# Kernel optimization log

Hardware: AMD Instinct MI355X
Metric: run time of the kernel (lower is better)

Reference implementation:

```python
import jax, jax.numpy as jnp
import numpy as np

D_MODEL = 1024
N_HEADS = 16
HEAD_DIM = D_MODEL // N_HEADS


def setup_inputs() -> dict:
    key = jax.random.key(0)
    ks = jax.random.split(key, 5)
    B, T = 2, 2048
    x = jax.random.normal(ks[0], (B, T, D_MODEL), dtype=jnp.float32)
    s_in = 1.0 / np.sqrt(D_MODEL)
    W_qkv = jax.random.normal(ks[1], (D_MODEL, 3 * D_MODEL), dtype=jnp.float32) * s_in
    b_qkv = jnp.zeros((3 * D_MODEL,), dtype=jnp.float32)
    W_out = jax.random.normal(ks[2], (D_MODEL, D_MODEL), dtype=jnp.float32) * s_in
    b_out = jnp.zeros((D_MODEL,), dtype=jnp.float32)
    return {"x": x, "W_qkv": W_qkv, "b_qkv": b_qkv, "W_out": W_out, "b_out": b_out}


def reference(x, W_qkv, b_qkv, W_out, b_out):
    B, T, C = x.shape
    qkv = x @ W_qkv + b_qkv  # (B, T, 3C)
    q, k, v = jnp.split(qkv, 3, axis=-1)
    # (B, H, T, Dh)
    q = q.reshape(B, T, N_HEADS, HEAD_DIM).transpose(0, 2, 1, 3)
    k = k.reshape(B, T, N_HEADS, HEAD_DIM).transpose(0, 2, 1, 3)
    v = v.reshape(B, T, N_HEADS, HEAD_DIM).transpose(0, 2, 1, 3)
    scale = 1.0 / jnp.sqrt(jnp.asarray(HEAD_DIM, dtype=x.dtype))
    scores = jnp.einsum('bhqd,bhkd->bhqk', q, k) * scale  # (B, H, T, T)
    causal = jnp.tril(jnp.ones((T, T), dtype=bool))
    scores = jnp.where(causal[None, None], scores, jnp.asarray(-jnp.inf, dtype=scores.dtype))
    attn = jax.nn.softmax(scores, axis=-1)
    out = jnp.einsum('bhqk,bhkd->bhqd', attn, v)  # (B, H, T, Dh)
    out = out.transpose(0, 2, 1, 3).reshape(B, T, C)
    return out @ W_out + b_out
```

## Files before the change

kernel.cpp:

```cpp
#include <hip/hip_runtime.h>
#include <hip/hip_bf16.h>
#include <stdint.h>

typedef __bf16 bf16;
typedef __bf16 bf16x4 __attribute__((ext_vector_type(4)));
typedef __bf16 bf16x8 __attribute__((ext_vector_type(8)));
typedef float  f32x4  __attribute__((ext_vector_type(4)));

#define D_MODEL 1024
#define N_HEADS 16
#define HEAD_DIM 64
#define SEQ 2048
#define BATCH 2
#define LOG2E 1.4426950408889634f
#define NEG_SENT -3.0e4f
#define CAP 24.0f

__device__ __forceinline__ bf16x8 ld8(const bf16* p) { return *(const bf16x8*)p; }

__device__ __forceinline__ void async16(const bf16* g, bf16* l) {
  __builtin_amdgcn_global_load_lds(
      (const __attribute__((address_space(1))) void*)g,
      (__attribute__((address_space(3))) void*)l, 16, 0, 0);
}

__global__ __launch_bounds__(256)
void prep(const float* __restrict__ x, bf16* __restrict__ x16,
          const float* __restrict__ Wqkv, bf16* __restrict__ Wqkv_t,
          const float* __restrict__ Wout, bf16* __restrict__ Wout_t) {
  __shared__ float tile[32][33];
  const int blk = blockIdx.x, tid = threadIdx.x;
  if (blk < 4096) {
    int i = (blk * 256 + tid) * 4;
    float4 v = *(const float4*)&x[i];
    bf16 o[4] = {(bf16)v.x, (bf16)v.y, (bf16)v.z, (bf16)v.w};
    *(uint2*)&x16[i] = *(uint2*)o;
    return;
  }
  const float* in; bf16* out; int R, C, c0, r0;
  if (blk < 7168) {
    int b = blk - 4096;
    in = Wqkv; out = Wqkv_t; R = 1024; C = 3072;
    c0 = (b % 96) * 32; r0 = (b / 96) * 32;
  } else {
    int b = blk - 7168;
    in = Wout; out = Wout_t; R = 1024; C = 1024;
    c0 = (b % 32) * 32; r0 = (b / 32) * 32;
  }
  const int tx = tid & 31, ty = tid >> 5;
  #pragma unroll
  for (int i = 0; i < 32; i += 8)
    tile[ty + i][tx] = in[(size_t)(r0 + ty + i) * C + c0 + tx];
  __syncthreads();
  #pragma unroll
  for (int i = 0; i < 32; i += 8)
    out[(size_t)(c0 + ty + i) * R + r0 + tx] = (bf16)tile[tx][ty + i];
}

__global__ __launch_bounds__(256)
void gemm_bt(const bf16* __restrict__ A, const bf16* __restrict__ Bt,
             const float* __restrict__ bias, float* __restrict__ outf,
             bf16* __restrict__ Qp, bf16* __restrict__ Kp, bf16* __restrict__ Vtp,
             int N, int mode) {
  __shared__ __align__(16) bf16 shA[128 * 32];
  __shared__ __align__(16) bf16 shB[128 * 32];
  const int tid  = threadIdx.x;
  const int bm0  = blockIdx.y * 128, bn0 = blockIdx.x * 128;
  const int wave = tid >> 6, lane = tid & 63;
  const int quad = lane >> 4, l16 = lane & 15;
  const int wm = (wave >> 1) * 64, wn = (wave & 1) * 64;

  const int c_lo  = tid;
  const int row_lo = c_lo >> 2,  col_lo = (c_lo & 3) << 3;
  const int c_hi  = tid + 256;
  const int row_hi = c_hi >> 2,  col_hi = (c_hi & 3) << 3;
  const int cb_lo = (wave * 64) * 8;
  const int cb_hi = (256 + wave * 64) * 8;

  f32x4 acc[4][4];
  #pragma unroll
  for (int i = 0; i < 4; i++)
    #pragma unroll
    for (int j = 0; j < 4; j++)
      acc[i][j] = (f32x4){0.f, 0.f, 0.f, 0.f};

  for (int k0 = 0; k0 < 1024; k0 += 32) {
    async16(&A[(size_t)(bm0 + row_lo) * 1024 + k0 + col_lo], &shA[cb_lo]);
    async16(&A[(size_t)(bm0 + row_hi) * 1024 + k0 + col_hi], &shA[cb_hi]);
    async16(&Bt[(size_t)(bn0 + row_lo) * 1024 + k0 + col_lo], &shB[cb_lo]);
    async16(&Bt[(size_t)(bn0 + row_hi) * 1024 + k0 + col_hi], &shB[cb_hi]);
    __syncthreads();
    bf16x8 af[4], bg[4];
    #pragma unroll
    for (int i = 0; i < 4; i++)
      af[i] = ld8(&shA[(wm + i * 16 + l16) * 32 + quad * 8]);
    #pragma unroll
    for (int j = 0; j < 4; j++)
      bg[j] = ld8(&shB[(wn + j * 16 + l16) * 32 + quad * 8]);
    #pragma unroll
    for (int i = 0; i < 4; i++)
      #pragma unroll
      for (int j = 0; j < 4; j++)
        acc[i][j] = __builtin_amdgcn_mfma_f32_16x16x32_bf16(af[i], bg[j], acc[i][j], 0, 0, 0);
    __syncthreads();
  }

  #pragma unroll
  for (int i = 0; i < 4; i++) {
    #pragma unroll
    for (int j = 0; j < 4; j++) {
      int gn = bn0 + wn + j * 16 + l16;
      float bv = bias[gn];
      #pragma unroll
      for (int r = 0; r < 4; r++) {
        int gm = bm0 + wm + i * 16 + quad * 4 + r;
        float v = acc[i][j][r] + bv;
        if (mode == 1) {
          outf[(size_t)gm * N + gn] = v;
        } else {
          int which = gn >> 10, rem = gn & 1023;
          int h = rem >> 6, d = rem & 63;
          int b = gm >> 11, t = gm & 2047;
          int bh = b * N_HEADS + h;
          if (which == 0)      Qp[((size_t)bh * SEQ + t) * 64 + d]  = (bf16)v;
          else if (which == 1) Kp[((size_t)bh * SEQ + t) * 64 + d]  = (bf16)v;
          else                 Vtp[((size_t)bh * 64 + d) * SEQ + t] = (bf16)v;
        }
      }
    }
  }
}

__global__ __launch_bounds__(256)
void attn_k(const bf16* __restrict__ Qp, const bf16* __restrict__ Kp,
            const bf16* __restrict__ Vtp, bf16* __restrict__ Obuf) {
  __shared__ __align__(16) bf16 shK[64 * 64];
  __shared__ __align__(16) bf16 shV[64 * 64];
  __shared__ __align__(16) bf16 shPT[4][16 * 72];
  const int tid  = threadIdx.x;
  const int wave = tid >> 6, lane = tid & 63;
  const int quad = lane >> 4, l16 = lane & 15;
  const int bh = blockIdx.y, bx = blockIdx.x;
  const int qb = (bx & 1) ? (31 - (bx >> 1)) : (bx >> 1);
  const int qw0 = qb * 64 + wave * 16;

  const bf16* Qbh = Qp  + (size_t)bh * SEQ * 64;
  const bf16* Kbh = Kp  + (size_t)bh * SEQ * 64;
  const bf16* Vbh = Vtp + (size_t)bh * 64 * SEQ;

  const int lr3 = lane >> 3;
  const int swc = (lane & 7) ^ lr3;

  bf16x8 aQ[2];
  #pragma unroll
  for (int p = 0; p < 2; p++)
    aQ[p] = ld8(&Qbh[(size_t)(qw0 + l16) * 64 + p * 32 + quad * 8]);

  f32x4 o[4];
  #pragma unroll
  for (int j = 0; j < 4; j++) o[j] = (f32x4){0.f, 0.f, 0.f, 0.f};
  f32x4 lacc = (f32x4){0.f, 0.f, 0.f, 0.f};
  const int qlane = qw0 + l16;
  const int xq = l16 & 7;

  const float SC = 0.125f * LOG2E;
  const int LT = qb;
  bf16* PT = shPT[wave];

  for (int kt = 0; kt <= LT; kt++) {
    const int kbase = kt * 64;
    __syncthreads();
    #pragma unroll
    for (int s = 0; s < 2; s++) {
      int i = wave * 2 + s;
      int row = i * 8 + lr3;
      async16(&Kbh[(size_t)(kbase + row) * 64 + swc * 8], &shK[i * 512]);
      async16(&Vbh[(size_t)row * SEQ + kbase + swc * 8], &shV[i * 512]);
    }
    __syncthreads();
    if (kbase > qw0 + 15) continue;

    f32x4 st[4];
    #pragma unroll
    for (int c = 0; c < 4; c++) {
      bf16x8 kf0 = ld8(&shK[(c * 16 + l16) * 64 + ((quad    ) ^ xq) * 8]);
      bf16x8 kf1 = ld8(&shK[(c * 16 + l16) * 64 + ((quad + 4) ^ xq) * 8]);
      f32x4 acc = (f32x4){0.f, 0.f, 0.f, 0.f};
      acc = __builtin_amdgcn_mfma_f32_16x16x32_bf16(kf0, aQ[0], acc, 0, 0, 0);
      acc = __builtin_amdgcn_mfma_f32_16x16x32_bf16(kf1, aQ[1], acc, 0, 0, 0);
      st[c] = acc;
    }

    if (kbase + 63 > qw0) {
      #pragma unroll
      for (int c = 0; c < 4; c++)
        #pragma unroll
        for (int r = 0; r < 4; r++) {
          int key = kbase + c * 16 + quad * 4 + r;
          if (key > qlane) st[c][r] = NEG_SENT;
        }
    }

    #pragma unroll
    for (int c = 0; c < 4; c++) {
      #pragma unroll
      for (int r = 0; r < 4; r++)
        st[c][r] = exp2f(__builtin_fmaf(st[c][r], SC, -CAP));
      lacc += st[c];
    }

    #pragma unroll
    for (int c = 0; c < 4; c++) {
      bf16x4 pv = {(bf16)st[c][0], (bf16)st[c][1], (bf16)st[c][2], (bf16)st[c][3]};
      *(bf16x4*)&PT[l16 * 72 + c * 16 + quad * 4] = pv;
    }
    asm volatile("s_waitcnt lgkmcnt(0)" ::: "memory");
    bf16x8 bP0 = ld8(&PT[l16 * 72 + quad * 8]);
    bf16x8 bP1 = ld8(&PT[l16 * 72 + 32 + quad * 8]);

    #pragma unroll
    for (int j = 0; j < 4; j++) {
      bf16x8 v0 = ld8(&shV[(j * 16 + l16) * 64 + ((quad    ) ^ xq) * 8]);
      bf16x8 v1 = ld8(&shV[(j * 16 + l16) * 64 + ((quad + 4) ^ xq) * 8]);
      o[j] = __builtin_amdgcn_mfma_f32_16x16x32_bf16(v0, bP0, o[j], 0, 0, 0);
      o[j] = __builtin_amdgcn_mfma_f32_16x16x32_bf16(v1, bP1, o[j], 0, 0, 0);
    }
  }

  float lrow = (lacc[0] + lacc[1]) + (lacc[2] + lacc[3]);
  lrow += __shfl_xor(lrow, 16, 64);
  lrow += __shfl_xor(lrow, 32, 64);

  const int b = bh >> 4, h = bh & 15;
  {
    float inv = 1.0f / lrow;
    int t = qw0 + l16;
    size_t base = ((size_t)(b * SEQ + t)) * D_MODEL + h * 64;
    #pragma unroll
    for (int j = 0; j < 4; j++) {
      bf16x4 ov = {(bf16)(o[j][0] * inv), (bf16)(o[j][1] * inv),
                   (bf16)(o[j][2] * inv), (bf16)(o[j][3] * inv)};
      *(bf16x4*)&Obuf[base + j * 16 + quad * 4] = ov;
    }
  }
}

extern "C" void kernel_launch(void* const* d_in, const int* in_sizes, int n_in,
                              void* d_out, int out_size, void* d_ws, size_t ws_size,
                              hipStream_t stream) {
  const float* x    = (const float*)d_in[0];
  const float* Wqkv = (const float*)d_in[1];
  const float* bqkv = (const float*)d_in[2];
  const float* Wout = (const float*)d_in[3];
  const float* bout = (const float*)d_in[4];
  float* out = (float*)d_out;

  char* ws = (char*)d_ws;
  bf16* x16    = (bf16*)(ws);
  bf16* Wqkv_t = (bf16*)(ws + 8388608);
  bf16* Wout_t = (bf16*)(ws + 14680064);
  bf16* Qp     = (bf16*)(ws + 16777216);
  bf16* Kp     = (bf16*)(ws + 25165824);
  bf16* Vtp    = (bf16*)(ws + 33554432);
  bf16* Obuf   = x16;

  prep<<<8192, 256, 0, stream>>>(x, x16, Wqkv, Wqkv_t, Wout, Wout_t);

  gemm_bt<<<dim3(3072 / 128, 4096 / 128), 256, 0, stream>>>(
      x16, Wqkv_t, bqkv, nullptr, Qp, Kp, Vtp, 3072, 0);

  attn_k<<<dim3(32, BATCH * N_HEADS), 256, 0, stream>>>(Qp, Kp, Vtp, Obuf);

  gemm_bt<<<dim3(1024 / 128, 4096 / 128), 256, 0, stream>>>(
      Obuf, Wout_t, bout, out, nullptr, nullptr, nullptr, 1024, 1);
}
```

Before: 220.6 us.

## Load 128-key K/V tiles per barrier pair and vectorize V-transpose epilogue stores

The attention kernel now stages 128 keys of K and V into shared memory per iteration and processes them as two 64-key halves. This halves the number of block-wide barrier pairs and global-to-LDS load rounds. The cost is doubled LDS use, which can lower occupancy, plus extra wasted loads on the diagonal tile. The QKV GEMM epilogue also writes the transposed V output as 4-wide bf16 vectors instead of scalar stores.

```diff
diff --git a/kernel.cpp b/kernel.cpp
--- a/kernel.cpp
+++ b/kernel.cpp
@@ -111,20 +111,25 @@
     for (int j = 0; j < 4; j++) {
       int gn = bn0 + wn + j * 16 + l16;
       float bv = bias[gn];
-      #pragma unroll
-      for (int r = 0; r < 4; r++) {
-        int gm = bm0 + wm + i * 16 + quad * 4 + r;
-        float v = acc[i][j][r] + bv;
-        if (mode == 1) {
-          outf[(size_t)gm * N + gn] = v;
+      int gm0 = bm0 + wm + i * 16 + quad * 4;
+      if (mode == 1) {
+        #pragma unroll
+        for (int r = 0; r < 4; r++)
+          outf[(size_t)(gm0 + r) * N + gn] = acc[i][j][r] + bv;
+      } else {
+        int which = gn >> 10, rem = gn & 1023;
+        int h = rem >> 6, d = rem & 63;
+        int b = gm0 >> 11, t0 = gm0 & 2047;
+        int bh = b * N_HEADS + h;
+        if (which == 2) {
+          bf16x4 vv = {(bf16)(acc[i][j][0] + bv), (bf16)(acc[i][j][1] + bv),
+                       (bf16)(acc[i][j][2] + bv), (bf16)(acc[i][j][3] + bv)};
+          *(bf16x4*)&Vtp[((size_t)bh * 64 + d) * SEQ + t0] = vv;
         } else {
-          int which = gn >> 10, rem = gn & 1023;
-          int h = rem >> 6, d = rem & 63;
-          int b = gm >> 11, t = gm & 2047;
-          int bh = b * N_HEADS + h;
-          if (which == 0)      Qp[((size_t)bh * SEQ + t) * 64 + d]  = (bf16)v;
-          else if (which == 1) Kp[((size_t)bh * SEQ + t) * 64 + d]  = (bf16)v;
-          else                 Vtp[((size_t)bh * 64 + d) * SEQ + t] = (bf16)v;
+          bf16* dst = (which == 0) ? Qp : Kp;
+          #pragma unroll
+          for (int r = 0; r < 4; r++)
+            dst[((size_t)bh * SEQ + t0 + r) * 64 + d] = (bf16)(acc[i][j][r] + bv);
         }
       }
     }
@@ -134,8 +139,8 @@
 __global__ __launch_bounds__(256)
 void attn_k(const bf16* __restrict__ Qp, const bf16* __restrict__ Kp,
             const bf16* __restrict__ Vtp, bf16* __restrict__ Obuf) {
-  __shared__ __align__(16) bf16 shK[64 * 64];
-  __shared__ __align__(16) bf16 shV[64 * 64];
+  __shared__ __align__(16) bf16 shK[128 * 64];
+  __shared__ __align__(16) bf16 shV[64 * 128];
   __shared__ __align__(16) bf16 shPT[4][16 * 72];
   const int tid  = threadIdx.x;
   const int wave = tid >> 6, lane = tid & 63;
@@ -148,9 +153,6 @@
   const bf16* Kbh = Kp  + (size_t)bh * SEQ * 64;
   const bf16* Vbh = Vtp + (size_t)bh * 64 * SEQ;
 
-  const int lr3 = lane >> 3;
-  const int swc = (lane & 7) ^ lr3;
-
   bf16x8 aQ[2];
   #pragma unroll
   for (int p = 0; p < 2; p++)
@@ -164,66 +166,81 @@
   const int xq = l16 & 7;
 
   const float SC = 0.125f * LOG2E;
-  const int LT = qb;
+  const int NT = qb >> 1;
   bf16* PT = shPT[wave];
 
-  for (int kt = 0; kt <= LT; kt++) {
-    const int kbase = kt * 64;
-    __syncthreads();
-    #pragma unroll
-    for (int s = 0; s < 2; s++) {
-      int i = wave * 2 + s;
-      int row = i * 8 + lr3;
-      async16(&Kbh[(size_t)(kbase + row) * 64 + swc * 8], &shK[i * 512]);
-      async16(&Vbh[(size_t)row * SEQ + kbase + swc * 8], &shV[i * 512]);
-    }
-    __syncthreads();
-    if (kbase > qw0 + 15) continue;
-
-    f32x4 st[4];
-    #pragma unroll
-    for (int c = 0; c < 4; c++) {
-      bf16x8 kf0 = ld8(&shK[(c * 16 + l16) * 64 + ((quad    ) ^ xq) * 8]);
-      bf16x8 kf1 = ld8(&shK[(c * 16 + l16) * 64 + ((quad + 4) ^ xq) * 8]);
-      f32x4 acc = (f32x4){0.f, 0.f, 0.f, 0.f};
-      acc = __builtin_amdgcn_mfma_f32_16x16x32_bf16(kf0, aQ[0], acc, 0, 0, 0);
-      acc = __builtin_amdgcn_mfma_f32_16x16x32_bf16(kf1, aQ[1], acc, 0, 0, 0);
-      st[c] = acc;
-    }
-
-    if (kbase + 63 > qw0) {
-      #pragma unroll
-      for (int c = 0; c < 4; c++)
+  for (int kt = 0; kt <= NT; kt++) {
+    const int kbase = kt * 128;
+    __syncthreads();
+    #pragma unroll
+    for (int s = 0; s < 4; s++) {
+      int id = tid + s * 256;
+      int kr = id >> 3, kc = id & 7;
+      async16(&Kbh[(size_t)(kbase + kr) * 64 + (kc ^ (kr & 7)) * 8], &shK[id * 8]);
+    }
+    #pragma unroll
+    for (int s = 0; s < 4; s++) {
+      int id = tid + s * 256;
+      int vd = id >> 4, vc = id & 15;
+      int svc = (vc & 8) | ((vc & 7) ^ (vd & 7));
+      async16(&Vbh[(size_t)vd * SEQ + kbase + svc * 8], &shV[id * 8]);
+    }
+    __syncthreads();
+
+    #pragma unroll
+    for (int h = 0; h < 2; h++) {
+      const int hb = kbase + h * 64;
+      if (hb > qw0 + 15) continue;
+
+      f32x4 st[4];
+      #pragma unroll
+      for (int c = 0; c < 4; c++) {
+        int kr0 = h * 64 + c * 16 + l16;
+        bf16x8 kf0 = ld8(&shK[kr0 * 64 + ((quad    ) ^ xq) * 8]);
+        bf16x8 kf1 = ld8(&shK[kr0 * 64 + ((quad + 4) ^ xq) * 8]);
+        f32x4 acc = (f32x4){0.f, 0.f, 0.f, 0.f};
+        acc = __builtin_amdgcn_mfma_f32_16x16x32_bf16(kf0, aQ[0], acc, 0, 0, 0);
+        acc = __builtin_amdgcn_mfma_f32_16x16x32_bf16(kf1, aQ[1], acc, 0, 0, 0);
+        st[c] = acc;
+      }
+
+      if (hb + 63 > qw0) {
         #pragma unroll
-        for (int r = 0; r < 4; r++) {
-          int key = kbase + c * 16 + quad * 4 + r;
-          if (key > qlane) st[c][r] = NEG_SENT;
-        }
-    }
-
-    #pragma unroll
-    for (int c = 0; c < 4; c++) {
-      #pragma unroll
-      for (int r = 0; r < 4; r++)
-        st[c][r] = exp2f(__builtin_fmaf(st[c][r], SC, -CAP));
-      lacc += st[c];
-    }
-
-    #pragma unroll
-    for (int c = 0; c < 4; c++) {
-      bf16x4 pv = {(bf16)st[c][0], (bf16)st[c][1], (bf16)st[c][2], (bf16)st[c][3]};
-      *(bf16x4*)&PT[l16 * 72 + c * 16 + quad * 4] = pv;
-    }
-    asm volatile("s_waitcnt lgkmcnt(0)" ::: "memory");
-    bf16x8 bP0 = ld8(&PT[l16 * 72 + quad * 8]);
-    bf16x8 bP1 = ld8(&PT[l16 * 72 + 32 + quad * 8]);
-
-    #pragma unroll
-    for (int j = 0; j < 4; j++) {
-      bf16x8 v0 = ld8(&shV[(j * 16 + l16) * 64 + ((quad    ) ^ xq) * 8]);
-      bf16x8 v1 = ld8(&shV[(j * 16 + l16) * 64 + ((quad + 4) ^ xq) * 8]);
-      o[j] = __builtin_amdgcn_mfma_f32_16x16x32_bf16(v0, bP0, o[j], 0, 0, 0);
-      o[j] = __builtin_amdgcn_mfma_f32_16x16x32_bf16(v1, bP1, o[j], 0, 0, 0);
+        for (int c = 0; c < 4; c++)
+          #pragma unroll
+          for (int r = 0; r < 4; r++) {
+            int key = hb + c * 16 + quad * 4 + r;
+            if (key > qlane) st[c][r] = NEG_SENT;
+          }
+      }
+
+      #pragma unroll
+      for (int c = 0; c < 4; c++) {
+        #pragma unroll
+        for (int r = 0; r < 4; r++)
+          st[c][r] = exp2f(__builtin_fmaf(st[c][r], SC, -CAP));
+        lacc += st[c];
+      }
+
+      if (h == 1)
+        asm volatile("s_waitcnt lgkmcnt(0)" ::: "memory");
+      #pragma unroll
+      for (int c = 0; c < 4; c++) {
+        bf16x4 pv = {(bf16)st[c][0], (bf16)st[c][1], (bf16)st[c][2], (bf16)st[c][3]};
+        *(bf16x4*)&PT[l16 * 72 + c * 16 + quad * 4] = pv;
+      }
+      asm volatile("s_waitcnt lgkmcnt(0)" ::: "memory");
+      bf16x8 bP0 = ld8(&PT[l16 * 72 + quad * 8]);
+      bf16x8 bP1 = ld8(&PT[l16 * 72 + 32 + quad * 8]);
+
+      #pragma unroll
+      for (int j = 0; j < 4; j++) {
+        int d = j * 16 + l16;
+        bf16x8 v0 = ld8(&shV[d * 128 + ((h * 8) | ((quad    ) ^ xq)) * 8]);
+        bf16x8 v1 = ld8(&shV[d * 128 + ((h * 8) | ((quad + 4) ^ xq)) * 8]);
+        o[j] = __builtin_amdgcn_mfma_f32_16x16x32_bf16(v0, bP0, o[j], 0, 0, 0);
+        o[j] = __builtin_amdgcn_mfma_f32_16x16x32_bf16(v1, bP1, o[j], 0, 0, 0);
+      }
     }
   }
 
```

New measurement: 217.6 us. No clear change (-1.3%).

## Double-buffer K/V tiles in attention and vectorize V-transpose epilogue stores

Applied to the files above, without the earlier changes.

The attention kernel now keeps two LDS buffers for K and V and issues the async loads for the next key tile before computing on the current one. This removes one barrier per iteration and hides global-to-LDS latency behind the MFMA and exp work. The QKV GEMM epilogue writes the transposed V as 4-element bf16 vectors along the sequence and hoists the per-row index math. The cost is doubled K/V shared memory, which may reduce occupancy.

```diff
diff --git a/kernel.cpp b/kernel.cpp
--- a/kernel.cpp
+++ b/kernel.cpp
@@ -111,20 +111,25 @@
     for (int j = 0; j < 4; j++) {
       int gn = bn0 + wn + j * 16 + l16;
       float bv = bias[gn];
-      #pragma unroll
-      for (int r = 0; r < 4; r++) {
-        int gm = bm0 + wm + i * 16 + quad * 4 + r;
-        float v = acc[i][j][r] + bv;
-        if (mode == 1) {
-          outf[(size_t)gm * N + gn] = v;
+      int gm0 = bm0 + wm + i * 16 + quad * 4;
+      if (mode == 1) {
+        #pragma unroll
+        for (int r = 0; r < 4; r++)
+          outf[(size_t)(gm0 + r) * N + gn] = acc[i][j][r] + bv;
+      } else {
+        int which = gn >> 10, rem = gn & 1023;
+        int h = rem >> 6, d = rem & 63;
+        int b = gm0 >> 11, t0 = gm0 & 2047;
+        int bh = b * N_HEADS + h;
+        if (which == 2) {
+          bf16x4 vv = {(bf16)(acc[i][j][0] + bv), (bf16)(acc[i][j][1] + bv),
+                       (bf16)(acc[i][j][2] + bv), (bf16)(acc[i][j][3] + bv)};
+          *(bf16x4*)&Vtp[((size_t)bh * 64 + d) * SEQ + t0] = vv;
         } else {
-          int which = gn >> 10, rem = gn & 1023;
-          int h = rem >> 6, d = rem & 63;
-          int b = gm >> 11, t = gm & 2047;
-          int bh = b * N_HEADS + h;
-          if (which == 0)      Qp[((size_t)bh * SEQ + t) * 64 + d]  = (bf16)v;
-          else if (which == 1) Kp[((size_t)bh * SEQ + t) * 64 + d]  = (bf16)v;
-          else                 Vtp[((size_t)bh * 64 + d) * SEQ + t] = (bf16)v;
+          bf16* dst = (which == 0) ? Qp : Kp;
+          #pragma unroll
+          for (int r = 0; r < 4; r++)
+            dst[((size_t)bh * SEQ + t0 + r) * 64 + d] = (bf16)(acc[i][j][r] + bv);
         }
       }
     }
@@ -134,8 +139,8 @@
 __global__ __launch_bounds__(256)
 void attn_k(const bf16* __restrict__ Qp, const bf16* __restrict__ Kp,
             const bf16* __restrict__ Vtp, bf16* __restrict__ Obuf) {
-  __shared__ __align__(16) bf16 shK[64 * 64];
-  __shared__ __align__(16) bf16 shV[64 * 64];
+  __shared__ __align__(16) bf16 shK[2][64 * 64];
+  __shared__ __align__(16) bf16 shV[2][64 * 64];
   __shared__ __align__(16) bf16 shPT[4][16 * 72];
   const int tid  = threadIdx.x;
   const int wave = tid >> 6, lane = tid & 63;
@@ -167,64 +172,83 @@
   const int LT = qb;
   bf16* PT = shPT[wave];
 
+  #pragma unroll
+  for (int s = 0; s < 2; s++) {
+    int i = wave * 2 + s;
+    int row = i * 8 + lr3;
+    async16(&Kbh[(size_t)row * 64 + swc * 8], &shK[0][i * 512]);
+    async16(&Vbh[(size_t)row * SEQ + swc * 8], &shV[0][i * 512]);
+  }
+  __syncthreads();
+
   for (int kt = 0; kt <= LT; kt++) {
     const int kbase = kt * 64;
+    const int buf = kt & 1;
+
+    if (kt < LT) {
+      const int nb = kbase + 64;
+      const int nbuf = buf ^ 1;
+      #pragma unroll
+      for (int s = 0; s < 2; s++) {
+        int i = wave * 2 + s;
+        int row = i * 8 + lr3;
+        async16(&Kbh[(size_t)(nb + row) * 64 + swc * 8], &shK[nbuf][i * 512]);
+        async16(&Vbh[(size_t)row * SEQ + nb + swc * 8], &shV[nbuf][i * 512]);
+      }
+    }
+
+    if (kbase <= qw0 + 15) {
+      const bf16* sK = shK[buf];
+      const bf16* sV = shV[buf];
+
+      f32x4 st[4];
+      #pragma unroll
+      for (int c = 0; c < 4; c++) {
+        bf16x8 kf0 = ld8(&sK[(c * 16 + l16) * 64 + ((quad    ) ^ xq) * 8]);
+        bf16x8 kf1 = ld8(&sK[(c * 16 + l16) * 64 + ((quad + 4) ^ xq) * 8]);
+        f32x4 acc = (f32x4){0.f, 0.f, 0.f, 0.f};
+        acc = __builtin_amdgcn_mfma_f32_16x16x32_bf16(kf0, aQ[0], acc, 0, 0, 0);
+        acc = __builtin_amdgcn_mfma_f32_16x16x32_bf16(kf1, aQ[1], acc, 0, 0, 0);
+        st[c] = acc;
+      }
+
+      if (kbase + 63 > qw0) {
+        #pragma unroll
+        for (int c = 0; c < 4; c++)
+          #pragma unroll
+          for (int r = 0; r < 4; r++) {
+            int key = kbase + c * 16 + quad * 4 + r;
+            if (key > qlane) st[c][r] = NEG_SENT;
+          }
+      }
+
+      #pragma unroll
+      for (int c = 0; c < 4; c++) {
+        #pragma unroll
+        for (int r = 0; r < 4; r++)
+          st[c][r] = exp2f(__builtin_fmaf(st[c][r], SC, -CAP));
+        lacc += st[c];
+      }
+
+      #pragma unroll
+      for (int c = 0; c < 4; c++) {
+        bf16x4 pv = {(bf16)st[c][0], (bf16)st[c][1], (bf16)st[c][2], (bf16)st[c][3]};
+        *(bf16x4*)&PT[l16 * 72 + c * 16 + quad * 4] = pv;
+      }
+      asm volatile("s_waitcnt lgkmcnt(0)" ::: "memory");
+      bf16x8 bP0 = ld8(&PT[l16 * 72 + quad * 8]);
+      bf16x8 bP1 = ld8(&PT[l16 * 72 + 32 + quad * 8]);
+
+      #pragma unroll
+      for (int j = 0; j < 4; j++) {
+        bf16x8 v0 = ld8(&sV[(j * 16 + l16) * 64 + ((quad    ) ^ xq) * 8]);
+        bf16x8 v1 = ld8(&sV[(j * 16 + l16) * 64 + ((quad + 4) ^ xq) * 8]);
+        o[j] = __builtin_amdgcn_mfma_f32_16x16x32_bf16(v0, bP0, o[j], 0, 0, 0);
+        o[j] = __builtin_amdgcn_mfma_f32_16x16x32_bf16(v1, bP1, o[j], 0, 0, 0);
+      }
+    }
+
     __syncthreads();
-    #pragma unroll
-    for (int s = 0; s < 2; s++) {
-      int i = wave * 2 + s;
-      int row = i * 8 + lr3;
-      async16(&Kbh[(size_t)(kbase + row) * 64 + swc * 8], &shK[i * 512]);
-      async16(&Vbh[(size_t)row * SEQ + kbase + swc * 8], &shV[i * 512]);
-    }
-    __syncthreads();
-    if (kbase > qw0 + 15) continue;
-
-    f32x4 st[4];
-    #pragma unroll
-    for (int c = 0; c < 4; c++) {
-      bf16x8 kf0 = ld8(&shK[(c * 16 + l16) * 64 + ((quad    ) ^ xq) * 8]);
-      bf16x8 kf1 = ld8(&shK[(c * 16 + l16) * 64 + ((quad + 4) ^ xq) * 8]);
-      f32x4 acc = (f32x4){0.f, 0.f, 0.f, 0.f};
-      acc = __builtin_amdgcn_mfma_f32_16x16x32_bf16(kf0, aQ[0], acc, 0, 0, 0);
-      acc = __builtin_amdgcn_mfma_f32_16x16x32_bf16(kf1, aQ[1], acc, 0, 0, 0);
-      st[c] = acc;
-    }
-
-    if (kbase + 63 > qw0) {
-      #pragma unroll
-      for (int c = 0; c < 4; c++)
-        #pragma unroll
-        for (int r = 0; r < 4; r++) {
-          int key = kbase + c * 16 + quad * 4 + r;
-          if (key > qlane) st[c][r] = NEG_SENT;
-        }
-    }
-
-    #pragma unroll
-    for (int c = 0; c < 4; c++) {
-      #pragma unroll
-      for (int r = 0; r < 4; r++)
-        st[c][r] = exp2f(__builtin_fmaf(st[c][r], SC, -CAP));
-      lacc += st[c];
-    }
-
-    #pragma unroll
-    for (int c = 0; c < 4; c++) {
-      bf16x4 pv = {(bf16)st[c][0], (bf16)st[c][1], (bf16)st[c][2], (bf16)st[c][3]};
-      *(bf16x4*)&PT[l16 * 72 + c * 16 + quad * 4] = pv;
-    }
-    asm volatile("s_waitcnt lgkmcnt(0)" ::: "memory");
-    bf16x8 bP0 = ld8(&PT[l16 * 72 + quad * 8]);
-    bf16x8 bP1 = ld8(&PT[l16 * 72 + 32 + quad * 8]);
-
-    #pragma unroll
-    for (int j = 0; j < 4; j++) {
-      bf16x8 v0 = ld8(&shV[(j * 16 + l16) * 64 + ((quad    ) ^ xq) * 8]);
-      bf16x8 v1 = ld8(&shV[(j * 16 + l16) * 64 + ((quad + 4) ^ xq) * 8]);
-      o[j] = __builtin_amdgcn_mfma_f32_16x16x32_bf16(v0, bP0, o[j], 0, 0, 0);
-      o[j] = __builtin_amdgcn_mfma_f32_16x16x32_bf16(v1, bP1, o[j], 0, 0, 0);
-    }
   }
 
   float lrow = (lacc[0] + lacc[1]) + (lacc[2] + lacc[3]);
```

Result: no change. 223.4 us (+1.3%).
